# Performance work log

Hardware: AMD Instinct MI355X
Metric: run time of the kernel (lower is better)

## Reference

```python
import jax, jax.numpy as jnp
import numpy as np

PI = np.pi

def dct_2_1d(x):
    # DCT-II over last dim, norm=None, matching the torch FFT-based impl.
    N = x.shape[-1]
    v = jnp.concatenate([x[..., ::2], jnp.flip(x[..., 1::2], axis=-1)], axis=-1)
    Vc = jnp.fft.fft(v, axis=-1)
    k = -jnp.arange(N, dtype=x.dtype) * PI / (2 * N)
    V = Vc.real * jnp.cos(k) - Vc.imag * jnp.sin(k)
    return 2 * V

def idct_2_1d(X):
    # Inverse of dct_2_1d (scaled DCT-III), norm=None.
    N = X.shape[-1]
    X_v = X / 2
    k = jnp.arange(N, dtype=X.dtype) * PI / (2 * N)
    W_r, W_i = jnp.cos(k), jnp.sin(k)
    V_t_r = X_v
    V_t_i = jnp.concatenate([jnp.zeros_like(X_v[..., :1]), -jnp.flip(X_v, axis=-1)[..., :-1]], axis=-1)
    V_r = V_t_r * W_r - V_t_i * W_i
    V_i = V_t_r * W_i + V_t_i * W_r
    # torch.fft.irfft(complex, n=N) uses the first N//2+1 entries; numpy/jax irfft crops the same way.
    v = jnp.fft.irfft(V_r + 1j * V_i, n=N, axis=-1)
    x = jnp.zeros_like(v)
    x = x.at[..., ::2].set(v[..., :N - N // 2])
    x = x.at[..., 1::2].set(jnp.flip(v, axis=-1)[..., :N // 2])
    return x

def setup_inputs() -> dict:
    key = jax.random.key(0)
    k1, k2 = jax.random.split(key)
    B, N, C = 256, 196, 768  # N = h*w = 14*14, C = dim
    x = jax.random.normal(k1, (B, N, C), dtype=jnp.float32)
    weight = jax.random.normal(k2, (C, N), dtype=jnp.float32) * 0.02
    return {"x": x, "weight": weight}

def reference(x, weight):
    # x: [B, N, C]; weight: [C, N]
    xt = jnp.transpose(x, (0, 2, 1)).astype(jnp.float32)  # [B, C, N]
    X = dct_2_1d(xt)
    X = X * weight  # broadcast [C, N] over batch
    y = idct_2_1d(X)
    return jnp.transpose(y, (0, 2, 1))  # [B, N, C]
```

## Files before the change

kernel.cpp:

```cpp
#include <hip/hip_runtime.h>

typedef __bf16 bf16;
typedef __bf16 bf16x8 __attribute__((ext_vector_type(8)));
typedef __bf16 bf16x4 __attribute__((ext_vector_type(4)));
typedef float f32x4 __attribute__((ext_vector_type(4)));

#define N_DIM 196
#define C_DIM 768
#define B_DIM 256
#define KSTEPS 7
#define MT1 14
#define MT2 13
#define CT 64
#define NTILES 12

#define D2F_ELEMS (MT1 * KSTEPS * 512)
#define EF_ELEMS  (MT2 * KSTEPS * 512)
#define WF_ELEMS  (NTILES * MT1 * 4 * 64 * 4)

__device__ __forceinline__ int swz(int row, int off) {
    return row * 256 + ((((off >> 3) ^ ((row >> 2) & 7) ^ ((row & 1) << 2)) << 3) | (off & 7));
}

__global__ void init_mats(const float* __restrict__ wgt,
                          bf16* __restrict__ d2f, bf16* __restrict__ ef,
                          float* __restrict__ wf) {
    int idx = blockIdx.x * 256 + threadIdx.x;
    const float PI = 3.14159265358979323846f;
    if (idx < D2F_ELEMS) {
        int j    = idx & 7;
        int lane = (idx >> 3) & 63;
        int rest = idx >> 9;
        int ks = rest % KSTEPS;
        int mt = rest / KSTEPS;
        int row = mt * 16 + (lane & 15);
        int col = ks * 32 + (lane >> 4) * 8 + j;
        float v = 0.0f;
        if (row < N_DIM && col < N_DIM) {
            int t = ((2 * col + 1) * row) % (4 * N_DIM);
            v = 2.0f * cosf(PI * (float)t / (float)(2 * N_DIM));
        }
        d2f[idx] = (bf16)v;
        return;
    }
    idx -= D2F_ELEMS;
    if (idx < EF_ELEMS) {
        int j    = idx & 7;
        int lane = (idx >> 3) & 63;
        int rest = idx >> 9;
        int ks = rest % KSTEPS;
        int mt = rest / KSTEPS;
        int row = mt * 16 + (lane & 15);
        int col = ks * 32 + (lane >> 4) * 8 + j;
        float v = 0.0f;
        if (row < N_DIM && col < N_DIM) {
            if (col == 0) v = 1.0f / (float)(2 * N_DIM);
            else {
                int t = ((2 * row + 1) * col) % (4 * N_DIM);
                v = cosf(PI * (float)t / (float)(2 * N_DIM)) / (float)N_DIM;
            }
        }
        ef[idx] = (bf16)v;
        return;
    }
    idx -= EF_ELEMS;
    if (idx < WF_ELEMS) {
        int r    = idx & 3;
        int lane = (idx >> 2) & 63;
        int rest = idx >> 8;
        int ct    = rest & 3;
        int rest2 = rest >> 2;
        int mt    = rest2 % MT1;
        int ctile = rest2 / MT1;
        int c = ctile * CT + ct * 16 + (lane & 15);
        int k = mt * 16 + ((lane >> 4) & 3) * 4 + r;
        wf[idx] = (k < N_DIM) ? wgt[(size_t)c * N_DIM + k] : 0.0f;
    }
}

__global__ __launch_bounds__(256, 5) void dct_fused(
        const float* __restrict__ x, const float* __restrict__ wf,
        const bf16* __restrict__ d2f, const bf16* __restrict__ ef,
        float* __restrict__ out) {
    __shared__ bf16 lds[CT * 256];

    const int ctile = blockIdx.x;
    const int b  = blockIdx.y;
    const int c0 = ctile * CT;
    const int t  = threadIdx.x;
    const int wave = t >> 6;
    const int lane = t & 63;
    const int ln15 = lane & 15;
    const int q    = lane >> 4;

    {
        const int c4 = (t & 15) * 4;
        const int mq = t >> 4;
#pragma unroll
        for (int i = 0; i < 4; ++i) {
            int quad = i * 16 + mq;
            if (quad > 55) continue;
            int m0 = quad * 4;
            float4 v0, v1, v2, v3;
            if (quad <= 48) {
                const float* p = x + ((size_t)b * N_DIM + m0) * C_DIM + c0 + c4;
                v0 = *(const float4*)(p);
                v1 = *(const float4*)(p + C_DIM);
                v2 = *(const float4*)(p + 2 * C_DIM);
                v3 = *(const float4*)(p + 3 * C_DIM);
            } else {
                v0 = v1 = v2 = v3 = make_float4(0.f, 0.f, 0.f, 0.f);
            }
            const float rx[4] = {v0.x, v1.x, v2.x, v3.x};
            const float ry[4] = {v0.y, v1.y, v2.y, v3.y};
            const float rz[4] = {v0.z, v1.z, v2.z, v3.z};
            const float rw[4] = {v0.w, v1.w, v2.w, v3.w};
            const float* rows[4] = {rx, ry, rz, rw};
#pragma unroll
            for (int k = 0; k < 4; ++k) {
                bf16x4 pv;
                pv[0] = (bf16)rows[k][0];
                pv[1] = (bf16)rows[k][1];
                pv[2] = (bf16)rows[k][2];
                pv[3] = (bf16)rows[k][3];
                *(bf16x4*)(lds + swz(c4 + k, m0)) = pv;
            }
        }
    }
    __syncthreads();

    f32x4 acc[4][4] = {};
    for (int ks = 0; ks < KSTEPS; ++ks) {
        bf16x8 bfr[4];
#pragma unroll
        for (int ct = 0; ct < 4; ++ct)
            bfr[ct] = *(const bf16x8*)(lds + swz(ct * 16 + ln15, ks * 32 + q * 8));
#pragma unroll
        for (int ml = 0; ml < 4; ++ml) {
            int mt = wave + 4 * ml;
            if (mt < MT1) {
                bf16x8 afr = *(const bf16x8*)(d2f + ((size_t)(mt * KSTEPS + ks) * 64 + lane) * 8);
#pragma unroll
                for (int ct = 0; ct < 4; ++ct)
                    acc[ml][ct] = __builtin_amdgcn_mfma_f32_16x16x32_bf16(afr, bfr[ct], acc[ml][ct], 0, 0, 0);
            }
        }
    }
    __syncthreads();

#pragma unroll
    for (int ml = 0; ml < 4; ++ml) {
        int mt = wave + 4 * ml;
        if (mt >= MT1) continue;
        int kb = mt * 16 + q * 4;
#pragma unroll
        for (int ct = 0; ct < 4; ++ct) {
            int cc = ct * 16 + ln15;
            float4 wv = *(const float4*)(wf + ((size_t)((ctile * MT1 + mt) * 4 + ct) * 64 + lane) * 4);
            bf16x4 pv;
            pv[0] = (bf16)(acc[ml][ct][0] * wv.x);
            pv[1] = (bf16)(acc[ml][ct][1] * wv.y);
            pv[2] = (bf16)(acc[ml][ct][2] * wv.z);
            pv[3] = (bf16)(acc[ml][ct][3] * wv.w);
            *(bf16x4*)(lds + swz(cc, kb)) = pv;
        }
    }
    __syncthreads();

    f32x4 acc2[4][4] = {};
    for (int ks = 0; ks < KSTEPS; ++ks) {
        bf16x8 bfr[4];
#pragma unroll
        for (int ct = 0; ct < 4; ++ct)
            bfr[ct] = *(const bf16x8*)(lds + swz(ct * 16 + ln15, ks * 32 + q * 8));
#pragma unroll
        for (int ml = 0; ml < 4; ++ml) {
            int mt = wave + 4 * ml;
            if (mt < MT2) {
                bf16x8 afr = *(const bf16x8*)(ef + ((size_t)(mt * KSTEPS + ks) * 64 + lane) * 8);
#pragma unroll
                for (int ct = 0; ct < 4; ++ct)
                    acc2[ml][ct] = __builtin_amdgcn_mfma_f32_16x16x32_bf16(afr, bfr[ct], acc2[ml][ct], 0, 0, 0);
            }
        }
    }

#pragma unroll
    for (int ml = 0; ml < 4; ++ml) {
        int mt = wave + 4 * ml;
        if (mt >= MT2) continue;
#pragma unroll
        for (int ct = 0; ct < 4; ++ct) {
            int cc = ct * 16 + ln15;
#pragma unroll
            for (int r = 0; r < 4; ++r) {
                int n = mt * 16 + q * 4 + r;
                if (n < N_DIM)
                    out[((size_t)b * N_DIM + n) * C_DIM + c0 + cc] = acc2[ml][ct][r];
            }
        }
    }
}

extern "C" void kernel_launch(void* const* d_in, const int* in_sizes, int n_in,
                              void* d_out, int out_size, void* d_ws, size_t ws_size,
                              hipStream_t stream) {
    const float* x   = (const float*)d_in[0];
    const float* wgt = (const float*)d_in[1];
    float* out = (float*)d_out;

    bf16* d2f  = (bf16*)d_ws;
    bf16* ef   = d2f + D2F_ELEMS;
    float* wf  = (float*)(ef + EF_ELEMS);

    int tot = D2F_ELEMS + EF_ELEMS + WF_ELEMS;
    init_mats<<<(tot + 255) / 256, 256, 0, stream>>>(wgt, d2f, ef, wf);

    dim3 grid(NTILES, B_DIM);
    dct_fused<<<grid, 256, 0, stream>>>(x, wf, d2f, ef, out);
}
```

Baseline: 355.8 us.

## Process four batches per block with register prefetch of next batch input

Each block now loops over four batch elements instead of one. The next batch's x tile is loaded into registers in two halves while the two MFMA GEMM phases of the current batch run, then converted to bf16 and written to LDS at the top of the next iteration. This hides global load latency behind compute and amortizes block launch overhead. In exchange it uses more registers (launch bounds drop from 5 to 3 blocks per SM), adds an extra barrier per iteration, and cuts the grid by a factor of four, which may reduce parallelism.

```diff
diff --git a/kernel.cpp b/kernel.cpp
--- a/kernel.cpp
+++ b/kernel.cpp
@@ -13,6 +13,7 @@
 #define MT2 13
 #define CT 64
 #define NTILES 12
+#define NB 4
 
 #define D2F_ELEMS (MT1 * KSTEPS * 512)
 #define EF_ELEMS  (MT2 * KSTEPS * 512)
@@ -78,127 +79,161 @@
     }
 }
 
-__global__ __launch_bounds__(256, 5) void dct_fused(
+#define ISSUE_HALF(pf, h, bb)                                                   \
+    _Pragma("unroll")                                                           \
+    for (int i = 0; i < 2; ++i) {                                               \
+        int quad = ((h) * 2 + i) * 16 + mslot;                                  \
+        if (quad <= 48) {                                                       \
+            const float* p = x + ((size_t)(bb) * N_DIM + quad * 4) * C_DIM + c0 + c4; \
+            _Pragma("unroll")                                                   \
+            for (int r = 0; r < 4; ++r)                                         \
+                pf[i][r] = *(const f32x4*)(p + r * C_DIM);                      \
+        }                                                                       \
+    }
+
+#define PACK_HALF(pk, pf, h)                                                    \
+    _Pragma("unroll")                                                           \
+    for (int i = 0; i < 2; ++i) {                                               \
+        int quad = ((h) * 2 + i) * 16 + mslot;                                  \
+        bool valid = (quad <= 48);                                              \
+        _Pragma("unroll")                                                       \
+        for (int j = 0; j < 4; ++j) {                                           \
+            bf16x4 v;                                                           \
+            v[0] = valid ? (bf16)pf[i][0][j] : (bf16)0.0f;                      \
+            v[1] = valid ? (bf16)pf[i][1][j] : (bf16)0.0f;                      \
+            v[2] = valid ? (bf16)pf[i][2][j] : (bf16)0.0f;                      \
+            v[3] = valid ? (bf16)pf[i][3][j] : (bf16)0.0f;                      \
+            pk[i][j] = v;                                                       \
+        }                                                                       \
+    }
+
+#define WRITE_HALF(pk, h)                                                       \
+    _Pragma("unroll")                                                           \
+    for (int i = 0; i < 2; ++i) {                                               \
+        int quad = ((h) * 2 + i) * 16 + mslot;                                  \
+        if (quad <= 55) {                                                       \
+            _Pragma("unroll")                                                   \
+            for (int j = 0; j < 4; ++j)                                         \
+                *(bf16x4*)(lds + swz(c4 + j, quad * 4)) = pk[i][j];             \
+        }                                                                       \
+    }
+
+__global__ __launch_bounds__(256, 3) void dct_fused(
         const float* __restrict__ x, const float* __restrict__ wf,
         const bf16* __restrict__ d2f, const bf16* __restrict__ ef,
         float* __restrict__ out) {
     __shared__ bf16 lds[CT * 256];
 
     const int ctile = blockIdx.x;
-    const int b  = blockIdx.y;
+    const int b0 = blockIdx.y * NB;
     const int c0 = ctile * CT;
     const int t  = threadIdx.x;
     const int wave = t >> 6;
     const int lane = t & 63;
     const int ln15 = lane & 15;
     const int q    = lane >> 4;
-
-    {
-        const int c4 = (t & 15) * 4;
-        const int mq = t >> 4;
-#pragma unroll
-        for (int i = 0; i < 4; ++i) {
-            int quad = i * 16 + mq;
-            if (quad > 55) continue;
-            int m0 = quad * 4;
-            float4 v0, v1, v2, v3;
-            if (quad <= 48) {
-                const float* p = x + ((size_t)b * N_DIM + m0) * C_DIM + c0 + c4;
-                v0 = *(const float4*)(p);
-                v1 = *(const float4*)(p + C_DIM);
-                v2 = *(const float4*)(p + 2 * C_DIM);
-                v3 = *(const float4*)(p + 3 * C_DIM);
-            } else {
-                v0 = v1 = v2 = v3 = make_float4(0.f, 0.f, 0.f, 0.f);
-            }
-            const float rx[4] = {v0.x, v1.x, v2.x, v3.x};
-            const float ry[4] = {v0.y, v1.y, v2.y, v3.y};
-            const float rz[4] = {v0.z, v1.z, v2.z, v3.z};
-            const float rw[4] = {v0.w, v1.w, v2.w, v3.w};
-            const float* rows[4] = {rx, ry, rz, rw};
-#pragma unroll
-            for (int k = 0; k < 4; ++k) {
-                bf16x4 pv;
-                pv[0] = (bf16)rows[k][0];
-                pv[1] = (bf16)rows[k][1];
-                pv[2] = (bf16)rows[k][2];
-                pv[3] = (bf16)rows[k][3];
-                *(bf16x4*)(lds + swz(c4 + k, m0)) = pv;
-            }
-        }
-    }
-    __syncthreads();
-
-    f32x4 acc[4][4] = {};
-    for (int ks = 0; ks < KSTEPS; ++ks) {
-        bf16x8 bfr[4];
-#pragma unroll
-        for (int ct = 0; ct < 4; ++ct)
-            bfr[ct] = *(const bf16x8*)(lds + swz(ct * 16 + ln15, ks * 32 + q * 8));
+    const int mslot = t >> 4;
+    const int c4    = (t & 15) * 4;
+
+    f32x4 pfa[2][4], pfb[2][4];
+    bf16x4 pka[2][4], pkb[2][4];
+
+    ISSUE_HALF(pfa, 0, b0)
+    ISSUE_HALF(pfb, 1, b0)
+    PACK_HALF(pka, pfa, 0)
+    PACK_HALF(pkb, pfb, 1)
+
+    for (int it = 0; it < NB; ++it) {
+        const int b = b0 + it;
+        const bool more = (it + 1 < NB);
+
+        WRITE_HALF(pka, 0)
+        WRITE_HALF(pkb, 1)
+        __syncthreads();
+
+        if (more) { ISSUE_HALF(pfa, 0, b + 1) }
+
+        f32x4 acc[4][4] = {};
+#pragma unroll
+        for (int ks = 0; ks < KSTEPS; ++ks) {
+            bf16x8 bfr0 = *(const bf16x8*)(lds + swz(0 * 16 + ln15, ks * 32 + q * 8));
+            bf16x8 bfr1 = *(const bf16x8*)(lds + swz(1 * 16 + ln15, ks * 32 + q * 8));
+            bf16x8 bfr2 = *(const bf16x8*)(lds + swz(2 * 16 + ln15, ks * 32 + q * 8));
+            bf16x8 bfr3 = *(const bf16x8*)(lds + swz(3 * 16 + ln15, ks * 32 + q * 8));
+#pragma unroll
+            for (int ml = 0; ml < 4; ++ml) {
+                int mt = wave + 4 * ml;
+                if (mt < MT1) {
+                    bf16x8 afr = *(const bf16x8*)(d2f + ((size_t)(mt * KSTEPS + ks) * 64 + lane) * 8);
+                    acc[ml][0] = __builtin_amdgcn_mfma_f32_16x16x32_bf16(afr, bfr0, acc[ml][0], 0, 0, 0);
+                    acc[ml][1] = __builtin_amdgcn_mfma_f32_16x16x32_bf16(afr, bfr1, acc[ml][1], 0, 0, 0);
+                    acc[ml][2] = __builtin_amdgcn_mfma_f32_16x16x32_bf16(afr, bfr2, acc[ml][2], 0, 0, 0);
+                    acc[ml][3] = __builtin_amdgcn_mfma_f32_16x16x32_bf16(afr, bfr3, acc[ml][3], 0, 0, 0);
+                }
+            }
+        }
+
+        if (more) { PACK_HALF(pka, pfa, 0) }
+        __syncthreads();
+
 #pragma unroll
         for (int ml = 0; ml < 4; ++ml) {
             int mt = wave + 4 * ml;
-            if (mt < MT1) {
-                bf16x8 afr = *(const bf16x8*)(d2f + ((size_t)(mt * KSTEPS + ks) * 64 + lane) * 8);
-#pragma unroll
-                for (int ct = 0; ct < 4; ++ct)
-                    acc[ml][ct] = __builtin_amdgcn_mfma_f32_16x16x32_bf16(afr, bfr[ct], acc[ml][ct], 0, 0, 0);
-            }
-        }
-    }
-    __syncthreads();
-
-#pragma unroll
-    for (int ml = 0; ml < 4; ++ml) {
-        int mt = wave + 4 * ml;
-        if (mt >= MT1) continue;
-        int kb = mt * 16 + q * 4;
-#pragma unroll
-        for (int ct = 0; ct < 4; ++ct) {
-            int cc = ct * 16 + ln15;
-            float4 wv = *(const float4*)(wf + ((size_t)((ctile * MT1 + mt) * 4 + ct) * 64 + lane) * 4);
-            bf16x4 pv;
-            pv[0] = (bf16)(acc[ml][ct][0] * wv.x);
-            pv[1] = (bf16)(acc[ml][ct][1] * wv.y);
-            pv[2] = (bf16)(acc[ml][ct][2] * wv.z);
-            pv[3] = (bf16)(acc[ml][ct][3] * wv.w);
-            *(bf16x4*)(lds + swz(cc, kb)) = pv;
-        }
-    }
-    __syncthreads();
-
-    f32x4 acc2[4][4] = {};
-    for (int ks = 0; ks < KSTEPS; ++ks) {
-        bf16x8 bfr[4];
-#pragma unroll
-        for (int ct = 0; ct < 4; ++ct)
-            bfr[ct] = *(const bf16x8*)(lds + swz(ct * 16 + ln15, ks * 32 + q * 8));
+            if (mt >= MT1) continue;
+            int kb = mt * 16 + q * 4;
+#pragma unroll
+            for (int ct = 0; ct < 4; ++ct) {
+                int cc = ct * 16 + ln15;
+                f32x4 wv = *(const f32x4*)(wf + ((size_t)((ctile * MT1 + mt) * 4 + ct) * 64 + lane) * 4);
+                bf16x4 pv;
+                pv[0] = (bf16)(acc[ml][ct][0] * wv[0]);
+                pv[1] = (bf16)(acc[ml][ct][1] * wv[1]);
+                pv[2] = (bf16)(acc[ml][ct][2] * wv[2]);
+                pv[3] = (bf16)(acc[ml][ct][3] * wv[3]);
+                *(bf16x4*)(lds + swz(cc, kb)) = pv;
+            }
+        }
+        __syncthreads();
+
+        if (more) { ISSUE_HALF(pfb, 1, b + 1) }
+
+        f32x4 acc2[4][4] = {};
+#pragma unroll
+        for (int ks = 0; ks < KSTEPS; ++ks) {
+            bf16x8 bfr0 = *(const bf16x8*)(lds + swz(0 * 16 + ln15, ks * 32 + q * 8));
+            bf16x8 bfr1 = *(const bf16x8*)(lds + swz(1 * 16 + ln15, ks * 32 + q * 8));
+            bf16x8 bfr2 = *(const bf16x8*)(lds + swz(2 * 16 + ln15, ks * 32 + q * 8));
+            bf16x8 bfr3 = *(const bf16x8*)(lds + swz(3 * 16 + ln15, ks * 32 + q * 8));
+#pragma unroll
+            for (int ml = 0; ml < 4; ++ml) {
+                int mt = wave + 4 * ml;
+                if (mt < MT2) {
+                    bf16x8 afr = *(const bf16x8*)(ef + ((size_t)(mt * KSTEPS + ks) * 64 + lane) * 8);
+                    acc2[ml][0] = __builtin_amdgcn_mfma_f32_16x16x32_bf16(afr, bfr0, acc2[ml][0], 0, 0, 0);
+                    acc2[ml][1] = __builtin_amdgcn_mfma_f32_16x16x32_bf16(afr, bfr1, acc2[ml][1], 0, 0, 0);
+                    acc2[ml][2] = __builtin_amdgcn_mfma_f32_16x16x32_bf16(afr, bfr2, acc2[ml][2], 0, 0, 0);
+                    acc2[ml][3] = __builtin_amdgcn_mfma_f32_16x16x32_bf16(afr, bfr3, acc2[ml][3], 0, 0, 0);
+                }
+            }
+        }
+
+        if (more) { PACK_HALF(pkb, pfb, 1) }
 #pragma unroll
         for (int ml = 0; ml < 4; ++ml) {
             int mt = wave + 4 * ml;
-            if (mt < MT2) {
-                bf16x8 afr = *(const bf16x8*)(ef + ((size_t)(mt * KSTEPS + ks) * 64 + lane) * 8);
-#pragma unroll
-                for (int ct = 0; ct < 4; ++ct)
-                    acc2[ml][ct] = __builtin_amdgcn_mfma_f32_16x16x32_bf16(afr, bfr[ct], acc2[ml][ct], 0, 0, 0);
-            }
-        }
-    }
-
-#pragma unroll
-    for (int ml = 0; ml < 4; ++ml) {
-        int mt = wave + 4 * ml;
-        if (mt >= MT2) continue;
-#pragma unroll
-        for (int ct = 0; ct < 4; ++ct) {
-            int cc = ct * 16 + ln15;
-#pragma unroll
-            for (int r = 0; r < 4; ++r) {
-                int n = mt * 16 + q * 4 + r;
-                if (n < N_DIM)
-                    out[((size_t)b * N_DIM + n) * C_DIM + c0 + cc] = acc2[ml][ct][r];
-            }
-        }
+            if (mt >= MT2) continue;
+#pragma unroll
+            for (int ct = 0; ct < 4; ++ct) {
+                int cc = ct * 16 + ln15;
+#pragma unroll
+                for (int r = 0; r < 4; ++r) {
+                    int n = mt * 16 + q * 4 + r;
+                    if (n < N_DIM)
+                        out[((size_t)b * N_DIM + n) * C_DIM + c0 + cc] = acc2[ml][ct][r];
+                }
+            }
+        }
+        __syncthreads();
     }
 }
 
@@ -211,11 +246,11 @@
 
     bf16* d2f  = (bf16*)d_ws;
     bf16* ef   = d2f + D2F_ELEMS;
-    float* wf  = (float*)(ef + EF_ELEMS);
+    float* wfp = (float*)(ef + EF_ELEMS);
 
     int tot = D2F_ELEMS + EF_ELEMS + WF_ELEMS;
-    init_mats<<<(tot + 255) / 256, 256, 0, stream>>>(wgt, d2f, ef, wf);
-
-    dim3 grid(NTILES, B_DIM);
-    dct_fused<<<grid, 256, 0, stream>>>(x, wf, d2f, ef, out);
-}
+    init_mats<<<(tot + 255) / 256, 256, 0, stream>>>(wgt, d2f, ef, wfp);
+
+    dim3 grid(NTILES, B_DIM / NB);
+    dct_fused<<<grid, 256, 0, stream>>>(x, wfp, d2f, ef, out);
+}
```

Result: slower. 517.3 us (+45.4%).
